# Kernel optimization log

Measured on AMD Instinct MI355X. Metric: run time of the kernel, lower is better.

Reference implementation:

```python
import jax, jax.numpy as jnp
import numpy as np

EPS = 1e-7        # min norm to avoid div-by-zero
BALL_EPS = 1e-5   # Poincare-ball boundary clip


def _norm(x):
    return jnp.maximum(jnp.linalg.norm(x, axis=-1, keepdims=True), EPS)


def expmap0(u, c):
    sc = jnp.sqrt(c)
    n = _norm(u)
    return jnp.tanh(sc * n) * u / (sc * n)


def logmap0(p, c):
    sc = jnp.sqrt(c)
    n = _norm(p)
    return jnp.arctanh(jnp.minimum(sc * n, 1.0 - BALL_EPS)) * p / (sc * n)


def proj(x, c):
    # project onto the ball of radius (1-eps)/sqrt(c)
    n = _norm(x)
    maxn = (1.0 - BALL_EPS) / jnp.sqrt(c)
    return jnp.where(n > maxn, x * (maxn / n), x)


def mobius_matvec(W, x, c):
    # Mobius matrix-vector multiply on the Poincare ball
    sc = jnp.sqrt(c)
    xn = _norm(x)                       # [N,1]
    mx = x @ W                          # [N,D]
    mxn = _norm(mx)
    t = jnp.tanh((mxn / xn) * jnp.arctanh(jnp.minimum(sc * xn, 1.0 - BALL_EPS)))
    return t * mx / (sc * mxn)


def spmm(rows, cols, vals, x):
    # sparse(adj) @ x, adjacency in COO form
    return jax.ops.segment_sum(vals[:, None] * x[cols], rows, num_segments=x.shape[0])


def hgc_layer(x, rows, cols, vals, W, c, c_lin):
    t = logmap0(x, c)                               # to tangent space at origin
    h = proj(mobius_matvec(W, t, c_lin), c_lin)     # LinearHyperbolic (c=1.0, no activation)
    s = spmm(rows, cols, vals, h)                   # HyperbolicAggregation: adj @ h
    agg = proj(expmap0(s, c), c)
    a = jax.nn.relu(logmap0(agg, c))                # ActivationHyperbolic (relu, c_in=c_out=c)
    return proj(expmap0(a, c), c)


def setup_inputs() -> dict:
    key = jax.random.key(0)
    ks = jax.random.split(key, 7)
    N, D, E = 10000, 1433, 100000
    x = jax.random.normal(ks[0], (N, D), jnp.float32) * 0.1  # keep points off the boundary
    rows = jax.random.randint(ks[1], (E,), 0, N)
    cols = jax.random.randint(ks[2], (E,), 0, N)
    vals = jax.random.uniform(ks[3], (E,), jnp.float32) / 10.0  # ~normalized adjacency weights
    scale = 1.0 / np.sqrt(D)
    W0 = jax.random.normal(ks[4], (D, D), jnp.float32) * scale
    W1 = jax.random.normal(ks[5], (D, D), jnp.float32) * scale
    W2 = jax.random.normal(ks[6], (D, D), jnp.float32) * scale
    return {"x": x, "W0": W0, "W1": W1, "W2": W2, "vals": vals, "rows": rows, "cols": cols}


def reference(x, W0, W1, W2, vals, rows, cols):
    c = jnp.float32(0.4)       # c_map == c0 for every layer in the source
    c_lin = jnp.float32(1.0)   # LinearHyperbolic hard-coded c
    h = expmap0(x, c)
    for W in (W0, W1, W2):
        h = hgc_layer(h, rows, cols, vals, W, c, c_lin)
    return h
```

## Files before the change

### kernel.cpp

```cpp
#include <hip/hip_runtime.h>

typedef unsigned short u16;
typedef unsigned int   u32;

#define M_ROWS 10000
#define D_DIM  1433
#define KPAD   1472
#define NPAD   1536
#define MPAD   10240
#define N_EDGE 100000
#define HPAD   1440
#define HP32   720
#define NKT    23
#define EPS    1e-7f
#define BEPS   1e-5f
#define SC     0.6324555320336759f

typedef __bf16 bf16x8 __attribute__((ext_vector_type(8)));
typedef float  f32x4  __attribute__((ext_vector_type(4)));
typedef u32    u32x4  __attribute__((ext_vector_type(4)));

__device__ __forceinline__ u16 f2bf(float f) {
  union { float f; unsigned u; } v; v.f = f;
  unsigned r = v.u + 0x7FFFu + ((v.u >> 16) & 1u);
  return (u16)(r >> 16);
}
__device__ __forceinline__ u32 pack2bf(float lo, float hi) {
  return (u32)f2bf(lo) | ((u32)f2bf(hi) << 16);
}
__device__ __forceinline__ float bflo(u32 u) { return __uint_as_float(u << 16); }
__device__ __forceinline__ float bfhi(u32 u) { return __uint_as_float(u & 0xFFFF0000u); }

__device__ __forceinline__ float atanh_f(float y) {
  return 0.5f * logf((1.f + y) / (1.f - y));
}

__device__ __forceinline__ void gl_lds16(const u16* g, u16* l) {
  __builtin_amdgcn_global_load_lds((const __attribute__((address_space(1))) void*)(const void*)g,
                                   (__attribute__((address_space(3))) void*)(void*)l,
                                   16, 0, 0);
}

__global__ __launch_bounds__(512, 1) void gemm256(
    const u16* __restrict__ A,
    const u16* __restrict__ B,
    u16* __restrict__ C,
    float* __restrict__ nrm)
{
  __shared__ u16 lds[2][2][256 * 64];

  const int tid  = threadIdx.x;
  const int lane = tid & 63;
  const int w    = tid >> 6;
  const int wr   = w >> 2;
  const int wc   = w & 3;

  const int flat = blockIdx.x;
  const int wgid = (flat & 7) * 30 + (flat >> 3);
  const int gy = wgid % 6;
  const int gx = wgid / 6;
  const long arow0 = (long)gx * 256;
  const long brow0 = (long)gy * 256;

  f32x4 acc[8][4] = {};

  const int sr8 = lane >> 3;
  const int scb = ((lane & 7) << 4) ^ (sr8 << 4);

  auto STG_B = [&](int b, int kt) {
    const long k0 = (long)kt * 64 + (scb >> 1);
#pragma unroll
    for (int l = 0; l < 4; ++l) {
      const int r   = l * 64 + w * 8 + sr8;
      const int dst = l * 4096 + w * 512;
      gl_lds16(B + (brow0 + r) * KPAD + k0, &lds[b][1][dst]);
    }
  };
  auto STG_A = [&](int b, int kt, int sel) {
    const long k0 = (long)kt * 64 + (scb >> 1);
#pragma unroll
    for (int li = 0; li < 2; ++li) {
      const int l   = sel + 2 * li;
      const int r   = l * 64 + w * 8 + sr8;
      const int dst = l * 4096 + w * 512;
      gl_lds16(A + (arow0 + r) * KPAD + k0, &lds[b][0][dst]);
    }
  };

  STG_B(0, 0); STG_A(0, 0, 0); STG_A(0, 0, 1);
  asm volatile("s_waitcnt vmcnt(0)" ::: "memory");
  __builtin_amdgcn_s_barrier();

  for (int kt = 0; kt < NKT; ++kt) {
    const int b = kt & 1;
    const bool pf = (kt + 1 < NKT);

    bf16x8 b0[4], b1[4], a0[4], a1[4];
#pragma unroll
    for (int ni = 0; ni < 4; ++ni) {
      const int row = wc * 64 + ni * 16 + (lane & 15);
      const int kb0 = (((lane >> 4) << 4)) ^ ((row & 7) << 4);
      const int kb1 = (64 + ((lane >> 4) << 4)) ^ ((row & 7) << 4);
      b0[ni] = *(const bf16x8*)&lds[b][1][row * 64 + (kb0 >> 1)];
      b1[ni] = *(const bf16x8*)&lds[b][1][row * 64 + (kb1 >> 1)];
    }
#pragma unroll
    for (int ml = 0; ml < 4; ++ml) {
      const int row = wr * 128 + ml * 16 + (lane & 15);
      const int kb0 = (((lane >> 4) << 4)) ^ ((row & 7) << 4);
      const int kb1 = (64 + ((lane >> 4) << 4)) ^ ((row & 7) << 4);
      a0[ml] = *(const bf16x8*)&lds[b][0][row * 64 + (kb0 >> 1)];
      a1[ml] = *(const bf16x8*)&lds[b][0][row * 64 + (kb1 >> 1)];
    }
    if (pf) { STG_B(b ^ 1, kt + 1); STG_A(b ^ 1, kt + 1, 0); }
    __builtin_amdgcn_s_setprio(1);
#pragma unroll
    for (int ml = 0; ml < 4; ++ml)
#pragma unroll
      for (int ni = 0; ni < 4; ++ni)
        acc[ml][ni] = __builtin_amdgcn_mfma_f32_16x16x32_bf16(a0[ml], b0[ni], acc[ml][ni], 0, 0, 0);
#pragma unroll
    for (int ml = 0; ml < 4; ++ml)
#pragma unroll
      for (int ni = 0; ni < 4; ++ni)
        acc[ml][ni] = __builtin_amdgcn_mfma_f32_16x16x32_bf16(a1[ml], b1[ni], acc[ml][ni], 0, 0, 0);
    __builtin_amdgcn_s_setprio(0);
    if (pf) asm volatile("s_waitcnt vmcnt(6)" ::: "memory");
    else    asm volatile("s_waitcnt vmcnt(0)" ::: "memory");
    __builtin_amdgcn_s_barrier();

    bf16x8 c0[4], c1[4];
#pragma unroll
    for (int ml = 0; ml < 4; ++ml) {
      const int row = wr * 128 + (4 + ml) * 16 + (lane & 15);
      const int kb0 = (((lane >> 4) << 4)) ^ ((row & 7) << 4);
      const int kb1 = (64 + ((lane >> 4) << 4)) ^ ((row & 7) << 4);
      c0[ml] = *(const bf16x8*)&lds[b][0][row * 64 + (kb0 >> 1)];
      c1[ml] = *(const bf16x8*)&lds[b][0][row * 64 + (kb1 >> 1)];
    }
    if (pf) STG_A(b ^ 1, kt + 1, 1);
    __builtin_amdgcn_s_setprio(1);
#pragma unroll
    for (int ml = 0; ml < 4; ++ml)
#pragma unroll
      for (int ni = 0; ni < 4; ++ni)
        acc[4 + ml][ni] = __builtin_amdgcn_mfma_f32_16x16x32_bf16(c0[ml], b0[ni], acc[4 + ml][ni], 0, 0, 0);
#pragma unroll
    for (int ml = 0; ml < 4; ++ml)
#pragma unroll
      for (int ni = 0; ni < 4; ++ni)
        acc[4 + ml][ni] = __builtin_amdgcn_mfma_f32_16x16x32_bf16(c1[ml], b1[ni], acc[4 + ml][ni], 0, 0, 0);
    __builtin_amdgcn_s_setprio(0);
    if (pf) asm volatile("s_waitcnt vmcnt(2)" ::: "memory");
    __builtin_amdgcn_s_barrier();
  }

  const int orw = (lane >> 4) * 4;
  const int ocl = lane & 15;

#pragma unroll
  for (int mi = 0; mi < 8; ++mi)
#pragma unroll
    for (int r = 0; r < 4; ++r) {
      float s = 0.f;
#pragma unroll
      for (int ni = 0; ni < 4; ++ni) {
        const long j = brow0 + wc * 64 + ni * 16 + ocl;
        const float v = acc[mi][ni][r];
        s += (j < D_DIM) ? v * v : 0.f;
      }
      s += __shfl_xor(s, 1, 64);
      s += __shfl_xor(s, 2, 64);
      s += __shfl_xor(s, 4, 64);
      s += __shfl_xor(s, 8, 64);
      if ((lane & 15) == 0)
        atomicAdd(&nrm[arow0 + wr * 128 + mi * 16 + orw + r], s);
    }

#pragma unroll
  for (int mi = 0; mi < 8; ++mi) {
    const long i0 = arow0 + wr * 128 + mi * 16 + orw;
    if (i0 >= M_ROWS) continue;
#pragma unroll
    for (int ni = 0; ni < 4; ++ni) {
      const long j = brow0 + wc * 64 + ni * 16 + ocl;
      if (j >= HPAD) continue;
#pragma unroll
      for (int r = 0; r < 4; ++r) {
        const long i = i0 + r;
        if (i < M_ROWS) C[i * HPAD + j] = (j < D_DIM) ? f2bf(acc[mi][ni][r]) : (u16)0;
      }
    }
  }
}

__device__ __forceinline__ float2 block_reduce2(float a, float b) {
  __shared__ float sa[4], sb[4];
#pragma unroll
  for (int off = 32; off > 0; off >>= 1) {
    a += __shfl_down(a, off, 64);
    b += __shfl_down(b, off, 64);
  }
  const int tid = threadIdx.x;
  if ((tid & 63) == 0) { sa[tid >> 6] = a; sb[tid >> 6] = b; }
  __syncthreads();
  const float ra = sa[0] + sa[1] + sa[2] + sa[3];
  const float rb = sb[0] + sb[1] + sb[2] + sb[3];
  __syncthreads();
  return make_float2(ra, rb);
}

__global__ __launch_bounds__(256) void pre_k(const float* __restrict__ x,
                                             u16* __restrict__ t,
                                             float* __restrict__ xn) {
  const long i = blockIdx.x;
  const int tid = threadIdx.x;
  u16* trow = t + i * KPAD;
  if (i >= M_ROWS) {
#pragma unroll
    for (int jj = 0; jj < 6; ++jj) { int j = tid + jj * 256; if (j < KPAD) trow[j] = 0; }
    return;
  }
  const float* xr = x + i * D_DIM;
  float v[6]; float s2 = 0.f;
#pragma unroll
  for (int jj = 0; jj < 6; ++jj) {
    int j = tid + jj * 256;
    v[jj] = (j < D_DIM) ? xr[j] : 0.f;
    s2 += v[jj] * v[jj];
  }
  s2 = block_reduce2(s2, 0.f).x;
  const float nx_t = sqrtf(s2);
  const float nx   = fmaxf(nx_t, EPS);
  const float al   = tanhf(SC * nx) / (SC * nx);
  const float n1   = fmaxf(al * nx_t, EPS);
  const float be   = atanh_f(fminf(SC * n1, 1.f - BEPS)) / (SC * n1);
  const float sca  = al * be;
  if (tid == 0) xn[i] = fmaxf(sca * nx_t, EPS);
#pragma unroll
  for (int jj = 0; jj < 6; ++jj) {
    int j = tid + jj * 256;
    if (j < KPAD) trow[j] = (j < D_DIM) ? f2bf(sca * v[jj]) : (u16)0;
  }
}

__global__ void zero_f(float* p, int n) {
  int i = blockIdx.x * 256 + threadIdx.x;
  if (i < n) p[i] = 0.f;
}

__global__ void fold_k(const int* __restrict__ ecol, const float* __restrict__ eval,
                       const float* __restrict__ nrm, const float* __restrict__ xn,
                       u32* __restrict__ pe, int E) {
  const int e = blockIdx.x * 256 + threadIdx.x;
  if (e >= E) return;
  const int c = ecol[e];
  const float realn = sqrtf(nrm[c]);
  const float mxn   = fmaxf(realn, EPS);
  const float xi    = xn[c];
  const float tf    = tanhf((mxn / xi) * atanh_f(fminf(xi, 1.f - BEPS)));
  float S = tf / mxn;
  const float hn = fmaxf(S * realn, EPS);
  const float maxn = 1.f - BEPS;
  if (hn > maxn) S *= maxn / hn;
  pe[e] = ((u32)c << 16) | (u32)f2bf(eval[e] * S);
}

__global__ __launch_bounds__(256) void spmm_post(const int* __restrict__ rp,
                                                 const u32* __restrict__ pe,
                                                 const u32* __restrict__ mxp,
                                                 u16* __restrict__ t,
                                                 float* __restrict__ xn,
                                                 float* __restrict__ out,
                                                 const int last) {
  const long r = blockIdx.x;
  const int tid = threadIdx.x;
  if (r >= M_ROWS) {
    if (!last && tid < 184) {
      u32* trow32 = (u32*)(t + r * KPAD);
#pragma unroll
      for (int k = 0; k < 4; ++k) trow32[4 * tid + k] = 0u;
    }
    return;
  }
  const bool act = tid < 180;
  const long boff = 4 * tid;
  float a[8] = {0.f, 0.f, 0.f, 0.f, 0.f, 0.f, 0.f, 0.f};
  const int e0 = rp[r], e1 = rp[r + 1];
  for (int e = e0; e < e1; e += 12) {
    u32 pp[12]; float w[12];
#pragma unroll
    for (int j = 0; j < 12; ++j) {
      const int ee = e + j;
      const int ec = (ee < e1) ? ee : (e1 - 1);
      pp[j] = pe[ec];
      w[j]  = (ee < e1) ? bflo(pp[j]) : 0.f;
    }
    if (act) {
      u32x4 q[12];
#pragma unroll
      for (int j = 0; j < 12; ++j)
        q[j] = *(const u32x4*)&mxp[(long)(pp[j] >> 16) * HP32 + boff];
#pragma unroll
      for (int j = 0; j < 12; ++j) {
#pragma unroll
        for (int k = 0; k < 4; ++k) {
          a[2 * k]     += w[j] * bflo(q[j][k]);
          a[2 * k + 1] += w[j] * bfhi(q[j][k]);
        }
      }
    }
  }
  float s2 = 0.f, s2p = 0.f;
#pragma unroll
  for (int k = 0; k < 8; ++k) {
    const int col = 8 * tid + k;
    const float v = (act && col < D_DIM) ? a[k] : 0.f;
    a[k] = v;
    s2 += v * v;
    const float p = fmaxf(v, 0.f);
    s2p += p * p;
  }
  const float2 red = block_reduce2(s2, s2p);
  const float ns_t  = sqrtf(red.x);
  const float nsp_t = sqrtf(red.y);
  const float maxn = (1.f - BEPS) / SC;
  const float ns = fmaxf(ns_t, EPS);
  const float al = tanhf(SC * ns) / (SC * ns);
  const float n1 = fmaxf(al * ns_t, EPS);
  const float be = (n1 > maxn) ? (maxn / n1) : 1.f;
  const float n2 = fmaxf(be * al * ns_t, EPS);
  const float lam = atanh_f(fminf(SC * n2, 1.f - BEPS)) / (SC * n2);
  const float g = lam * be * al;
  const float na_t = g * nsp_t;
  const float n3 = fmaxf(na_t, EPS);
  const float mu = tanhf(SC * n3) / (SC * n3);
  const float n4 = fmaxf(mu * na_t, EPS);
  const float nu = (n4 > maxn) ? (maxn / n4) : 1.f;
  const float T = nu * mu * g;
  if (last) {
    if (act) {
      float* orow = out + r * (long)D_DIM;
#pragma unroll
      for (int k = 0; k < 8; ++k) {
        const int col = 8 * tid + k;
        if (col < D_DIM) orow[col] = T * fmaxf(a[k], 0.f);
      }
    }
  } else {
    const float nh_t = T * nsp_t;
    const float n5 = fmaxf(nh_t, EPS);
    const float kap = atanh_f(fminf(SC * n5, 1.f - BEPS)) / (SC * n5);
    const float F = kap * T;
    if (tid == 0) xn[r] = fmaxf(F * nsp_t, EPS);
    u32* trow32 = (u32*)(t + r * KPAD);
    if (act) {
#pragma unroll
      for (int k = 0; k < 4; ++k)
        trow32[4 * tid + k] = pack2bf(F * fmaxf(a[2 * k], 0.f), F * fmaxf(a[2 * k + 1], 0.f));
    } else if (tid < 184) {
#pragma unroll
      for (int k = 0; k < 4; ++k) trow32[4 * tid + k] = 0u;
    }
  }
}

__global__ void wt_conv(const float* __restrict__ W, u16* __restrict__ Wt) {
  __shared__ float tile[32][33];
  const int kb = blockIdx.x * 32, nb = blockIdx.y * 32;
  const int tx = threadIdx.x, ty = threadIdx.y;
#pragma unroll
  for (int r = 0; r < 32; r += 8) {
    const int k = kb + ty + r, n = nb + tx;
    tile[ty + r][tx] = (k < D_DIM && n < D_DIM) ? W[(long)k * D_DIM + n] : 0.f;
  }
  __syncthreads();
#pragma unroll
  for (int r = 0; r < 32; r += 8) {
    const int n = nb + ty + r, k = kb + tx;
    if (n < NPAD && k < KPAD) Wt[(long)n * KPAD + k] = f2bf(tile[tx][ty + r]);
  }
}

__global__ void zero_int(int* p, int n) {
  int i = blockIdx.x * 256 + threadIdx.x;
  if (i < n) p[i] = 0;
}
__global__ void hist_k(const int* __restrict__ rows, int* __restrict__ counts, int E) {
  int e = blockIdx.x * 256 + threadIdx.x;
  if (e < E) atomicAdd(&counts[rows[e]], 1);
}
__global__ __launch_bounds__(1024) void scan_rp(const int* __restrict__ counts,
                                                int* __restrict__ rp, int n) {
  __shared__ int sd[1024];
  __shared__ int carry_s;
  const int tid = threadIdx.x;
  if (tid == 0) { carry_s = 0; rp[0] = 0; }
  __syncthreads();
  for (int base = 0; base < n; base += 1024) {
    const int i = base + tid;
    sd[tid] = (i < n) ? counts[i] : 0;
    __syncthreads();
    for (int off = 1; off < 1024; off <<= 1) {
      const int tv = (tid >= off) ? sd[tid - off] : 0;
      __syncthreads();
      sd[tid] += tv;
      __syncthreads();
    }
    const int carry = carry_s;
    if (i < n) rp[i + 1] = carry + sd[tid];
    __syncthreads();
    if (tid == 1023) carry_s = carry + sd[1023];
    __syncthreads();
  }
}
__global__ void scatter_k(const int* __restrict__ rows, const int* __restrict__ cols,
                          const float* __restrict__ vals, const int* __restrict__ rp,
                          int* __restrict__ cursor, int* __restrict__ ecol,
                          float* __restrict__ eval, int E) {
  int e = blockIdx.x * 256 + threadIdx.x;
  if (e < E) {
    const int r = rows[e];
    const int pos = rp[r] + atomicAdd(&cursor[r], 1);
    ecol[pos] = cols[e];
    eval[pos] = vals[e];
  }
}

extern "C" void kernel_launch(void* const* d_in, const int* in_sizes, int n_in,
                              void* d_out, int out_size, void* d_ws, size_t ws_size,
                              hipStream_t stream) {
  (void)in_sizes; (void)n_in; (void)out_size; (void)ws_size;
  const float* x    = (const float*)d_in[0];
  const float* W[3] = {(const float*)d_in[1], (const float*)d_in[2], (const float*)d_in[3]};
  const float* vals = (const float*)d_in[4];
  const int*   rows = (const int*)d_in[5];
  const int*   cols = (const int*)d_in[6];
  float* out = (float*)d_out;

  char* base = (char*)d_ws;
  size_t off = 0;
  auto take = [&](size_t bytes) {
    void* q = base + off;
    off = (off + bytes + 255) & ~(size_t)255;
    return q;
  };
  u16*   t    = (u16*)take((size_t)MPAD * KPAD * 2);
  u16*   Wt   = (u16*)take((size_t)NPAD * KPAD * 2);
  u16*   mx   = (u16*)take((size_t)M_ROWS * HPAD * 2);
  float* nrm3 = (float*)take((size_t)3 * MPAD * 4);
  float* xn   = (float*)take((size_t)M_ROWS * 4);
  int*   cnt  = (int*)take((size_t)M_ROWS * 2 * 4);
  int*   rp   = (int*)take((size_t)(M_ROWS + 1) * 4);
  int*   ecol = (int*)take((size_t)N_EDGE * 4);
  float* eval = (float*)take((size_t)N_EDGE * 4);
  u32*   pe   = (u32*)take((size_t)N_EDGE * 4);

  zero_int<<<(2 * M_ROWS + 255) / 256, 256, 0, stream>>>(cnt, 2 * M_ROWS);
  hist_k<<<(N_EDGE + 255) / 256, 256, 0, stream>>>(rows, cnt, N_EDGE);
  scan_rp<<<1, 1024, 0, stream>>>(cnt, rp, M_ROWS);
  scatter_k<<<(N_EDGE + 255) / 256, 256, 0, stream>>>(rows, cols, vals, rp,
                                                      cnt + M_ROWS, ecol, eval, N_EDGE);
  zero_f<<<(3 * MPAD + 255) / 256, 256, 0, stream>>>(nrm3, 3 * MPAD);

  pre_k<<<MPAD, 256, 0, stream>>>(x, t, xn);

  for (int L = 0; L < 3; ++L) {
    float* nrm = nrm3 + (size_t)L * MPAD;
    wt_conv<<<dim3(46, 48), dim3(32, 8), 0, stream>>>(W[L], Wt);
    gemm256<<<240, 512, 0, stream>>>(t, Wt, mx, nrm);
    fold_k<<<(N_EDGE + 255) / 256, 256, 0, stream>>>(ecol, eval, nrm, xn, pe, N_EDGE);
    spmm_post<<<MPAD, 256, 0, stream>>>(rp, pe, (const u32*)mx, t, xn, out, (L == 2) ? 1 : 0);
  }
}
```

Baseline: 369.5 us.

## Restructure GEMM main loop into four quadrant phases with two-stage-ahead prefetch

The GEMM k-loop now splits each 256x256 tile step into four MFMA quadrant phases. B and A loads are issued in half-tile pieces two k-steps ahead, reusing the current buffer as soon as its fragments have been read into registers, to hide global-load latency better than single-step double buffering. Separately, spmm_post now runs with 192 threads instead of 256, since only 180 threads do work, and the block reduction is templated on wave count. The tighter schedule adds more barriers and relies on vmcnt counts being exactly right, so a miscount could race on LDS.

```diff
diff --git a/kernel.cpp b/kernel.cpp
--- a/kernel.cpp
+++ b/kernel.cpp
@@ -41,6 +41,8 @@
                                    16, 0, 0);
 }
 
+#define BAR() asm volatile("s_barrier" ::: "memory")
+
 __global__ __launch_bounds__(512, 1) void gemm256(
     const u16* __restrict__ A,
     const u16* __restrict__ B,
@@ -66,93 +68,137 @@
 
   const int sr8 = lane >> 3;
   const int scb = ((lane & 7) << 4) ^ (sr8 << 4);
-
-  auto STG_B = [&](int b, int kt) {
-    const long k0 = (long)kt * 64 + (scb >> 1);
-#pragma unroll
-    for (int l = 0; l < 4; ++l) {
-      const int r   = l * 64 + w * 8 + sr8;
-      const int dst = l * 4096 + w * 512;
-      gl_lds16(B + (brow0 + r) * KPAD + k0, &lds[b][1][dst]);
-    }
-  };
+  const int l15 = lane & 15;
+  const int khi = (lane >> 4) << 4;
+
   auto STG_A = [&](int b, int kt, int sel) {
     const long k0 = (long)kt * 64 + (scb >> 1);
 #pragma unroll
     for (int li = 0; li < 2; ++li) {
-      const int l   = sel + 2 * li;
-      const int r   = l * 64 + w * 8 + sr8;
+      const int l = sel + 2 * li;
+      const int r = l * 64 + w * 8 + sr8;
       const int dst = l * 4096 + w * 512;
       gl_lds16(A + (arow0 + r) * KPAD + k0, &lds[b][0][dst]);
     }
   };
-
-  STG_B(0, 0); STG_A(0, 0, 0); STG_A(0, 0, 1);
-  asm volatile("s_waitcnt vmcnt(0)" ::: "memory");
-  __builtin_amdgcn_s_barrier();
+  auto STG_B = [&](int b, int kt, int half) {
+    const long k0 = (long)kt * 64 + (scb >> 1);
+#pragma unroll
+    for (int j = 0; j < 2; ++j) {
+      const int r128 = j * 64 + w * 8;
+      const int rb   = ((r128 >> 5) << 6) + half * 32 + (r128 & 31);
+      gl_lds16(B + (brow0 + rb + sr8) * KPAD + k0, &lds[b][1][rb * 64]);
+    }
+  };
+
+  STG_B(0, 0, 0); STG_A(0, 0, 0); STG_B(0, 0, 1); STG_A(0, 0, 1);
+  STG_A(1, 1, 0); STG_B(1, 1, 1); STG_A(1, 1, 1);
+  asm volatile("s_waitcnt vmcnt(6)" ::: "memory");
+  BAR();
 
   for (int kt = 0; kt < NKT; ++kt) {
     const int b = kt & 1;
-    const bool pf = (kt + 1 < NKT);
-
-    bf16x8 b0[4], b1[4], a0[4], a1[4];
-#pragma unroll
-    for (int ni = 0; ni < 4; ++ni) {
-      const int row = wc * 64 + ni * 16 + (lane & 15);
-      const int kb0 = (((lane >> 4) << 4)) ^ ((row & 7) << 4);
-      const int kb1 = (64 + ((lane >> 4) << 4)) ^ ((row & 7) << 4);
-      b0[ni] = *(const bf16x8*)&lds[b][1][row * 64 + (kb0 >> 1)];
-      b1[ni] = *(const bf16x8*)&lds[b][1][row * 64 + (kb1 >> 1)];
-    }
-#pragma unroll
-    for (int ml = 0; ml < 4; ++ml) {
-      const int row = wr * 128 + ml * 16 + (lane & 15);
-      const int kb0 = (((lane >> 4) << 4)) ^ ((row & 7) << 4);
-      const int kb1 = (64 + ((lane >> 4) << 4)) ^ ((row & 7) << 4);
-      a0[ml] = *(const bf16x8*)&lds[b][0][row * 64 + (kb0 >> 1)];
-      a1[ml] = *(const bf16x8*)&lds[b][0][row * 64 + (kb1 >> 1)];
-    }
-    if (pf) { STG_B(b ^ 1, kt + 1); STG_A(b ^ 1, kt + 1, 0); }
+    const bool s1 = (kt + 1 < NKT);
+    const bool s2 = (kt + 2 < NKT);
+
+    bf16x8 a0[4], a1[4], bl0[2], bl1[2];
+#pragma unroll
+    for (int mi = 0; mi < 4; ++mi) {
+      const int row = wr * 128 + mi * 16 + l15;
+      const int x0 = (khi) ^ ((row & 7) << 4);
+      const int x1 = (64 + khi) ^ ((row & 7) << 4);
+      a0[mi] = *(const bf16x8*)&lds[b][0][row * 64 + (x0 >> 1)];
+      a1[mi] = *(const bf16x8*)&lds[b][0][row * 64 + (x1 >> 1)];
+    }
+#pragma unroll
+    for (int ni = 0; ni < 2; ++ni) {
+      const int row = wc * 64 + ni * 16 + l15;
+      const int x0 = (khi) ^ ((row & 7) << 4);
+      const int x1 = (64 + khi) ^ ((row & 7) << 4);
+      bl0[ni] = *(const bf16x8*)&lds[b][1][row * 64 + (x0 >> 1)];
+      bl1[ni] = *(const bf16x8*)&lds[b][1][row * 64 + (x1 >> 1)];
+    }
+    if (s1) STG_B(b ^ 1, kt + 1, 0);
+    BAR();
     __builtin_amdgcn_s_setprio(1);
 #pragma unroll
-    for (int ml = 0; ml < 4; ++ml)
-#pragma unroll
-      for (int ni = 0; ni < 4; ++ni)
-        acc[ml][ni] = __builtin_amdgcn_mfma_f32_16x16x32_bf16(a0[ml], b0[ni], acc[ml][ni], 0, 0, 0);
-#pragma unroll
-    for (int ml = 0; ml < 4; ++ml)
-#pragma unroll
-      for (int ni = 0; ni < 4; ++ni)
-        acc[ml][ni] = __builtin_amdgcn_mfma_f32_16x16x32_bf16(a1[ml], b1[ni], acc[ml][ni], 0, 0, 0);
+    for (int mi = 0; mi < 4; ++mi)
+#pragma unroll
+      for (int ni = 0; ni < 2; ++ni)
+        acc[mi][ni] = __builtin_amdgcn_mfma_f32_16x16x32_bf16(a0[mi], bl0[ni], acc[mi][ni], 0, 0, 0);
+#pragma unroll
+    for (int mi = 0; mi < 4; ++mi)
+#pragma unroll
+      for (int ni = 0; ni < 2; ++ni)
+        acc[mi][ni] = __builtin_amdgcn_mfma_f32_16x16x32_bf16(a1[mi], bl1[ni], acc[mi][ni], 0, 0, 0);
     __builtin_amdgcn_s_setprio(0);
-    if (pf) asm volatile("s_waitcnt vmcnt(6)" ::: "memory");
-    else    asm volatile("s_waitcnt vmcnt(0)" ::: "memory");
-    __builtin_amdgcn_s_barrier();
-
-    bf16x8 c0[4], c1[4];
-#pragma unroll
-    for (int ml = 0; ml < 4; ++ml) {
-      const int row = wr * 128 + (4 + ml) * 16 + (lane & 15);
-      const int kb0 = (((lane >> 4) << 4)) ^ ((row & 7) << 4);
-      const int kb1 = (64 + ((lane >> 4) << 4)) ^ ((row & 7) << 4);
-      c0[ml] = *(const bf16x8*)&lds[b][0][row * 64 + (kb0 >> 1)];
-      c1[ml] = *(const bf16x8*)&lds[b][0][row * 64 + (kb1 >> 1)];
-    }
-    if (pf) STG_A(b ^ 1, kt + 1, 1);
+    BAR();
+
+    bf16x8 bh0[2], bh1[2];
+#pragma unroll
+    for (int ni = 0; ni < 2; ++ni) {
+      const int row = wc * 64 + (2 + ni) * 16 + l15;
+      const int x0 = (khi) ^ ((row & 7) << 4);
+      const int x1 = (64 + khi) ^ ((row & 7) << 4);
+      bh0[ni] = *(const bf16x8*)&lds[b][1][row * 64 + (x0 >> 1)];
+      bh1[ni] = *(const bf16x8*)&lds[b][1][row * 64 + (x1 >> 1)];
+    }
+    if (s2) STG_A(b, kt + 2, 0);
+    BAR();
     __builtin_amdgcn_s_setprio(1);
 #pragma unroll
-    for (int ml = 0; ml < 4; ++ml)
-#pragma unroll
-      for (int ni = 0; ni < 4; ++ni)
-        acc[4 + ml][ni] = __builtin_amdgcn_mfma_f32_16x16x32_bf16(c0[ml], b0[ni], acc[4 + ml][ni], 0, 0, 0);
-#pragma unroll
-    for (int ml = 0; ml < 4; ++ml)
-#pragma unroll
-      for (int ni = 0; ni < 4; ++ni)
-        acc[4 + ml][ni] = __builtin_amdgcn_mfma_f32_16x16x32_bf16(c1[ml], b1[ni], acc[4 + ml][ni], 0, 0, 0);
+    for (int mi = 0; mi < 4; ++mi)
+#pragma unroll
+      for (int ni = 0; ni < 2; ++ni)
+        acc[mi][2 + ni] = __builtin_amdgcn_mfma_f32_16x16x32_bf16(a0[mi], bh0[ni], acc[mi][2 + ni], 0, 0, 0);
+#pragma unroll
+    for (int mi = 0; mi < 4; ++mi)
+#pragma unroll
+      for (int ni = 0; ni < 2; ++ni)
+        acc[mi][2 + ni] = __builtin_amdgcn_mfma_f32_16x16x32_bf16(a1[mi], bh1[ni], acc[mi][2 + ni], 0, 0, 0);
     __builtin_amdgcn_s_setprio(0);
-    if (pf) asm volatile("s_waitcnt vmcnt(2)" ::: "memory");
-    __builtin_amdgcn_s_barrier();
+    BAR();
+
+#pragma unroll
+    for (int mi = 0; mi < 4; ++mi) {
+      const int row = wr * 128 + (4 + mi) * 16 + l15;
+      const int x0 = (khi) ^ ((row & 7) << 4);
+      const int x1 = (64 + khi) ^ ((row & 7) << 4);
+      a0[mi] = *(const bf16x8*)&lds[b][0][row * 64 + (x0 >> 1)];
+      a1[mi] = *(const bf16x8*)&lds[b][0][row * 64 + (x1 >> 1)];
+    }
+    if (s2) STG_B(b, kt + 2, 1);
+    BAR();
+    __builtin_amdgcn_s_setprio(1);
+#pragma unroll
+    for (int mi = 0; mi < 4; ++mi)
+#pragma unroll
+      for (int ni = 0; ni < 2; ++ni)
+        acc[4 + mi][2 + ni] = __builtin_amdgcn_mfma_f32_16x16x32_bf16(a0[mi], bh0[ni], acc[4 + mi][2 + ni], 0, 0, 0);
+#pragma unroll
+    for (int mi = 0; mi < 4; ++mi)
+#pragma unroll
+      for (int ni = 0; ni < 2; ++ni)
+        acc[4 + mi][2 + ni] = __builtin_amdgcn_mfma_f32_16x16x32_bf16(a1[mi], bh1[ni], acc[4 + mi][2 + ni], 0, 0, 0);
+    __builtin_amdgcn_s_setprio(0);
+    BAR();
+
+    if (s2) STG_A(b, kt + 2, 1);
+    __builtin_amdgcn_s_setprio(1);
+#pragma unroll
+    for (int mi = 0; mi < 4; ++mi)
+#pragma unroll
+      for (int ni = 0; ni < 2; ++ni)
+        acc[4 + mi][ni] = __builtin_amdgcn_mfma_f32_16x16x32_bf16(a0[mi], bl0[ni], acc[4 + mi][ni], 0, 0, 0);
+#pragma unroll
+    for (int mi = 0; mi < 4; ++mi)
+#pragma unroll
+      for (int ni = 0; ni < 2; ++ni)
+        acc[4 + mi][ni] = __builtin_amdgcn_mfma_f32_16x16x32_bf16(a1[mi], bl1[ni], acc[4 + mi][ni], 0, 0, 0);
+    __builtin_amdgcn_s_setprio(0);
+    if (s2)      asm volatile("s_waitcnt vmcnt(6)" ::: "memory");
+    else if (s1) asm volatile("s_waitcnt vmcnt(0)" ::: "memory");
+    BAR();
   }
 
   const int orw = (lane >> 4) * 4;
@@ -194,8 +240,9 @@
   }
 }
 
+template<int NW>
 __device__ __forceinline__ float2 block_reduce2(float a, float b) {
-  __shared__ float sa[4], sb[4];
+  __shared__ float sa[NW], sb[NW];
 #pragma unroll
   for (int off = 32; off > 0; off >>= 1) {
     a += __shfl_down(a, off, 64);
@@ -204,8 +251,9 @@
   const int tid = threadIdx.x;
   if ((tid & 63) == 0) { sa[tid >> 6] = a; sb[tid >> 6] = b; }
   __syncthreads();
-  const float ra = sa[0] + sa[1] + sa[2] + sa[3];
-  const float rb = sb[0] + sb[1] + sb[2] + sb[3];
+  float ra = 0.f, rb = 0.f;
+#pragma unroll
+  for (int i = 0; i < NW; ++i) { ra += sa[i]; rb += sb[i]; }
   __syncthreads();
   return make_float2(ra, rb);
 }
@@ -229,7 +277,7 @@
     v[jj] = (j < D_DIM) ? xr[j] : 0.f;
     s2 += v[jj] * v[jj];
   }
-  s2 = block_reduce2(s2, 0.f).x;
+  s2 = block_reduce2<4>(s2, 0.f).x;
   const float nx_t = sqrtf(s2);
   const float nx   = fmaxf(nx_t, EPS);
   const float al   = tanhf(SC * nx) / (SC * nx);
@@ -266,7 +314,7 @@
   pe[e] = ((u32)c << 16) | (u32)f2bf(eval[e] * S);
 }
 
-__global__ __launch_bounds__(256) void spmm_post(const int* __restrict__ rp,
+__global__ __launch_bounds__(192) void spmm_post(const int* __restrict__ rp,
                                                  const u32* __restrict__ pe,
                                                  const u32* __restrict__ mxp,
                                                  u16* __restrict__ t,
@@ -321,7 +369,7 @@
     const float p = fmaxf(v, 0.f);
     s2p += p * p;
   }
-  const float2 red = block_reduce2(s2, s2p);
+  const float2 red = block_reduce2<3>(s2, s2p);
   const float ns_t  = sqrtf(red.x);
   const float nsp_t = sqrtf(red.y);
   const float maxn = (1.f - BEPS) / SC;
@@ -470,6 +518,6 @@
     wt_conv<<<dim3(46, 48), dim3(32, 8), 0, stream>>>(W[L], Wt);
     gemm256<<<240, 512, 0, stream>>>(t, Wt, mx, nrm);
     fold_k<<<(N_EDGE + 255) / 256, 256, 0, stream>>>(ecol, eval, nrm, xn, pe, N_EDGE);
-    spmm_post<<<MPAD, 256, 0, stream>>>(rp, pe, (const u32*)mx, t, xn, out, (L == 2) ? 1 : 0);
-  }
-}
+    spmm_post<<<MPAD, 192, 0, stream>>>(rp, pe, (const u32*)mx, t, xn, out, (L == 2) ? 1 : 0);
+  }
+}
```

After: 376.3 us. No clear change (+1.9%).

## Interleave GEMM LDS reads with prefetch via sched groups; shrink spmm blocks to 192

Applied to the files above, without the earlier changes.

Restructures the GEMM main loop: the last k-tile is peeled out so the prefetch branches disappear, LDS fragment reads are split around the global-to-LDS prefetch issue, and sched_group_barrier hints are added to interleave DS reads, VMEM and MFMA. The aim is to hide LDS and global latency behind MFMA work. Separately, spmm_post now launches 192 threads instead of 256, since only 180 lanes were active, and the block reduction is templated on wave count. The scheduling hints may constrain the compiler poorly and raise register pressure.

```diff
diff --git a/kernel.cpp b/kernel.cpp
--- a/kernel.cpp
+++ b/kernel.cpp
@@ -41,6 +41,9 @@
                                    16, 0, 0);
 }
 
+#define BAR() asm volatile("s_barrier" ::: "memory")
+#define SGB(m, n) __builtin_amdgcn_sched_group_barrier((m), (n), 0)
+
 __global__ __launch_bounds__(512, 1) void gemm256(
     const u16* __restrict__ A,
     const u16* __restrict__ B,
@@ -66,6 +69,8 @@
 
   const int sr8 = lane >> 3;
   const int scb = ((lane & 7) << 4) ^ (sr8 << 4);
+  const int l15 = lane & 15;
+  const int khi = (lane >> 4) << 4;
 
   auto STG_B = [&](int b, int kt) {
     const long k0 = (long)kt * 64 + (scb >> 1);
@@ -89,70 +94,143 @@
 
   STG_B(0, 0); STG_A(0, 0, 0); STG_A(0, 0, 1);
   asm volatile("s_waitcnt vmcnt(0)" ::: "memory");
-  __builtin_amdgcn_s_barrier();
-
-  for (int kt = 0; kt < NKT; ++kt) {
+  BAR();
+
+  for (int kt = 0; kt < NKT - 1; ++kt) {
     const int b = kt & 1;
-    const bool pf = (kt + 1 < NKT);
-
-    bf16x8 b0[4], b1[4], a0[4], a1[4];
+
+    bf16x8 a0[4], a1[4], b0q[4], b1q[4];
 #pragma unroll
     for (int ni = 0; ni < 4; ++ni) {
-      const int row = wc * 64 + ni * 16 + (lane & 15);
-      const int kb0 = (((lane >> 4) << 4)) ^ ((row & 7) << 4);
-      const int kb1 = (64 + ((lane >> 4) << 4)) ^ ((row & 7) << 4);
-      b0[ni] = *(const bf16x8*)&lds[b][1][row * 64 + (kb0 >> 1)];
-      b1[ni] = *(const bf16x8*)&lds[b][1][row * 64 + (kb1 >> 1)];
+      const int row = wc * 64 + ni * 16 + l15;
+      const int x0 = (khi) ^ ((row & 7) << 4);
+      b0q[ni] = *(const bf16x8*)&lds[b][1][row * 64 + (x0 >> 1)];
     }
 #pragma unroll
     for (int ml = 0; ml < 4; ++ml) {
-      const int row = wr * 128 + ml * 16 + (lane & 15);
-      const int kb0 = (((lane >> 4) << 4)) ^ ((row & 7) << 4);
-      const int kb1 = (64 + ((lane >> 4) << 4)) ^ ((row & 7) << 4);
-      a0[ml] = *(const bf16x8*)&lds[b][0][row * 64 + (kb0 >> 1)];
-      a1[ml] = *(const bf16x8*)&lds[b][0][row * 64 + (kb1 >> 1)];
-    }
-    if (pf) { STG_B(b ^ 1, kt + 1); STG_A(b ^ 1, kt + 1, 0); }
+      const int row = wr * 128 + ml * 16 + l15;
+      const int x0 = (khi) ^ ((row & 7) << 4);
+      a0[ml] = *(const bf16x8*)&lds[b][0][row * 64 + (x0 >> 1)];
+    }
+    STG_B(b ^ 1, kt + 1);
+    STG_A(b ^ 1, kt + 1, 0);
+#pragma unroll
+    for (int ni = 0; ni < 4; ++ni) {
+      const int row = wc * 64 + ni * 16 + l15;
+      const int x1 = (64 + khi) ^ ((row & 7) << 4);
+      b1q[ni] = *(const bf16x8*)&lds[b][1][row * 64 + (x1 >> 1)];
+    }
+#pragma unroll
+    for (int ml = 0; ml < 4; ++ml) {
+      const int row = wr * 128 + ml * 16 + l15;
+      const int x1 = (64 + khi) ^ ((row & 7) << 4);
+      a1[ml] = *(const bf16x8*)&lds[b][0][row * 64 + (x1 >> 1)];
+    }
     __builtin_amdgcn_s_setprio(1);
 #pragma unroll
     for (int ml = 0; ml < 4; ++ml)
 #pragma unroll
       for (int ni = 0; ni < 4; ++ni)
-        acc[ml][ni] = __builtin_amdgcn_mfma_f32_16x16x32_bf16(a0[ml], b0[ni], acc[ml][ni], 0, 0, 0);
-#pragma unroll
-    for (int ml = 0; ml < 4; ++ml)
-#pragma unroll
-      for (int ni = 0; ni < 4; ++ni)
-        acc[ml][ni] = __builtin_amdgcn_mfma_f32_16x16x32_bf16(a1[ml], b1[ni], acc[ml][ni], 0, 0, 0);
+        acc[ml][ni] = __builtin_amdgcn_mfma_f32_16x16x32_bf16(a0[ml], b0q[ni], acc[ml][ni], 0, 0, 0);
+#pragma unroll
+    for (int ml = 0; ml < 4; ++ml)
+#pragma unroll
+      for (int ni = 0; ni < 4; ++ni)
+        acc[ml][ni] = __builtin_amdgcn_mfma_f32_16x16x32_bf16(a1[ml], b1q[ni], acc[ml][ni], 0, 0, 0);
     __builtin_amdgcn_s_setprio(0);
-    if (pf) asm volatile("s_waitcnt vmcnt(6)" ::: "memory");
-    else    asm volatile("s_waitcnt vmcnt(0)" ::: "memory");
-    __builtin_amdgcn_s_barrier();
+    SGB(0x100, 8);
+    SGB(0x010, 6);
+    SGB(0x008, 16);
+    SGB(0x100, 8);
+    SGB(0x008, 16);
+    asm volatile("s_waitcnt vmcnt(6)" ::: "memory");
+    BAR();
 
     bf16x8 c0[4], c1[4];
 #pragma unroll
     for (int ml = 0; ml < 4; ++ml) {
-      const int row = wr * 128 + (4 + ml) * 16 + (lane & 15);
-      const int kb0 = (((lane >> 4) << 4)) ^ ((row & 7) << 4);
-      const int kb1 = (64 + ((lane >> 4) << 4)) ^ ((row & 7) << 4);
-      c0[ml] = *(const bf16x8*)&lds[b][0][row * 64 + (kb0 >> 1)];
-      c1[ml] = *(const bf16x8*)&lds[b][0][row * 64 + (kb1 >> 1)];
-    }
-    if (pf) STG_A(b ^ 1, kt + 1, 1);
+      const int row = wr * 128 + (4 + ml) * 16 + l15;
+      const int x0 = (khi) ^ ((row & 7) << 4);
+      c0[ml] = *(const bf16x8*)&lds[b][0][row * 64 + (x0 >> 1)];
+    }
+    STG_A(b ^ 1, kt + 1, 1);
+#pragma unroll
+    for (int ml = 0; ml < 4; ++ml) {
+      const int row = wr * 128 + (4 + ml) * 16 + l15;
+      const int x1 = (64 + khi) ^ ((row & 7) << 4);
+      c1[ml] = *(const bf16x8*)&lds[b][0][row * 64 + (x1 >> 1)];
+    }
     __builtin_amdgcn_s_setprio(1);
 #pragma unroll
     for (int ml = 0; ml < 4; ++ml)
 #pragma unroll
       for (int ni = 0; ni < 4; ++ni)
-        acc[4 + ml][ni] = __builtin_amdgcn_mfma_f32_16x16x32_bf16(c0[ml], b0[ni], acc[4 + ml][ni], 0, 0, 0);
-#pragma unroll
-    for (int ml = 0; ml < 4; ++ml)
-#pragma unroll
-      for (int ni = 0; ni < 4; ++ni)
-        acc[4 + ml][ni] = __builtin_amdgcn_mfma_f32_16x16x32_bf16(c1[ml], b1[ni], acc[4 + ml][ni], 0, 0, 0);
+        acc[4 + ml][ni] = __builtin_amdgcn_mfma_f32_16x16x32_bf16(c0[ml], b0q[ni], acc[4 + ml][ni], 0, 0, 0);
+#pragma unroll
+    for (int ml = 0; ml < 4; ++ml)
+#pragma unroll
+      for (int ni = 0; ni < 4; ++ni)
+        acc[4 + ml][ni] = __builtin_amdgcn_mfma_f32_16x16x32_bf16(c1[ml], b1q[ni], acc[4 + ml][ni], 0, 0, 0);
     __builtin_amdgcn_s_setprio(0);
-    if (pf) asm volatile("s_waitcnt vmcnt(2)" ::: "memory");
-    __builtin_amdgcn_s_barrier();
+    SGB(0x100, 4);
+    SGB(0x010, 2);
+    SGB(0x008, 16);
+    SGB(0x100, 4);
+    SGB(0x008, 16);
+    asm volatile("s_waitcnt vmcnt(2)" ::: "memory");
+    BAR();
+  }
+
+  {
+    const int b = (NKT - 1) & 1;
+    bf16x8 a0[4], a1[4], b0q[4], b1q[4];
+#pragma unroll
+    for (int ni = 0; ni < 4; ++ni) {
+      const int row = wc * 64 + ni * 16 + l15;
+      const int x0 = (khi) ^ ((row & 7) << 4);
+      const int x1 = (64 + khi) ^ ((row & 7) << 4);
+      b0q[ni] = *(const bf16x8*)&lds[b][1][row * 64 + (x0 >> 1)];
+      b1q[ni] = *(const bf16x8*)&lds[b][1][row * 64 + (x1 >> 1)];
+    }
+#pragma unroll
+    for (int ml = 0; ml < 4; ++ml) {
+      const int row = wr * 128 + ml * 16 + l15;
+      const int x0 = (khi) ^ ((row & 7) << 4);
+      const int x1 = (64 + khi) ^ ((row & 7) << 4);
+      a0[ml] = *(const bf16x8*)&lds[b][0][row * 64 + (x0 >> 1)];
+      a1[ml] = *(const bf16x8*)&lds[b][0][row * 64 + (x1 >> 1)];
+    }
+#pragma unroll
+    for (int ml = 0; ml < 4; ++ml)
+#pragma unroll
+      for (int ni = 0; ni < 4; ++ni)
+        acc[ml][ni] = __builtin_amdgcn_mfma_f32_16x16x32_bf16(a0[ml], b0q[ni], acc[ml][ni], 0, 0, 0);
+#pragma unroll
+    for (int ml = 0; ml < 4; ++ml)
+#pragma unroll
+      for (int ni = 0; ni < 4; ++ni)
+        acc[ml][ni] = __builtin_amdgcn_mfma_f32_16x16x32_bf16(a1[ml], b1q[ni], acc[ml][ni], 0, 0, 0);
+    asm volatile("s_waitcnt vmcnt(0)" ::: "memory");
+    BAR();
+    bf16x8 c0[4], c1[4];
+#pragma unroll
+    for (int ml = 0; ml < 4; ++ml) {
+      const int row = wr * 128 + (4 + ml) * 16 + l15;
+      const int x0 = (khi) ^ ((row & 7) << 4);
+      const int x1 = (64 + khi) ^ ((row & 7) << 4);
+      c0[ml] = *(const bf16x8*)&lds[b][0][row * 64 + (x0 >> 1)];
+      c1[ml] = *(const bf16x8*)&lds[b][0][row * 64 + (x1 >> 1)];
+    }
+#pragma unroll
+    for (int ml = 0; ml < 4; ++ml)
+#pragma unroll
+      for (int ni = 0; ni < 4; ++ni)
+        acc[4 + ml][ni] = __builtin_amdgcn_mfma_f32_16x16x32_bf16(c0[ml], b0q[ni], acc[4 + ml][ni], 0, 0, 0);
+#pragma unroll
+    for (int ml = 0; ml < 4; ++ml)
+#pragma unroll
+      for (int ni = 0; ni < 4; ++ni)
+        acc[4 + ml][ni] = __builtin_amdgcn_mfma_f32_16x16x32_bf16(c1[ml], b1q[ni], acc[4 + ml][ni], 0, 0, 0);
   }
 
   const int orw = (lane >> 4) * 4;
@@ -194,8 +272,9 @@
   }
 }
 
+template<int NW>
 __device__ __forceinline__ float2 block_reduce2(float a, float b) {
-  __shared__ float sa[4], sb[4];
+  __shared__ float sa[NW], sb[NW];
 #pragma unroll
   for (int off = 32; off > 0; off >>= 1) {
     a += __shfl_down(a, off, 64);
@@ -204,8 +283,9 @@
   const int tid = threadIdx.x;
   if ((tid & 63) == 0) { sa[tid >> 6] = a; sb[tid >> 6] = b; }
   __syncthreads();
-  const float ra = sa[0] + sa[1] + sa[2] + sa[3];
-  const float rb = sb[0] + sb[1] + sb[2] + sb[3];
+  float ra = 0.f, rb = 0.f;
+#pragma unroll
+  for (int i = 0; i < NW; ++i) { ra += sa[i]; rb += sb[i]; }
   __syncthreads();
   return make_float2(ra, rb);
 }
@@ -229,7 +309,7 @@
     v[jj] = (j < D_DIM) ? xr[j] : 0.f;
     s2 += v[jj] * v[jj];
   }
-  s2 = block_reduce2(s2, 0.f).x;
+  s2 = block_reduce2<4>(s2, 0.f).x;
   const float nx_t = sqrtf(s2);
   const float nx   = fmaxf(nx_t, EPS);
   const float al   = tanhf(SC * nx) / (SC * nx);
@@ -266,7 +346,7 @@
   pe[e] = ((u32)c << 16) | (u32)f2bf(eval[e] * S);
 }
 
-__global__ __launch_bounds__(256) void spmm_post(const int* __restrict__ rp,
+__global__ __launch_bounds__(192) void spmm_post(const int* __restrict__ rp,
                                                  const u32* __restrict__ pe,
                                                  const u32* __restrict__ mxp,
                                                  u16* __restrict__ t,
@@ -321,7 +401,7 @@
     const float p = fmaxf(v, 0.f);
     s2p += p * p;
   }
-  const float2 red = block_reduce2(s2, s2p);
+  const float2 red = block_reduce2<3>(s2, s2p);
   const float ns_t  = sqrtf(red.x);
   const float nsp_t = sqrtf(red.y);
   const float maxn = (1.f - BEPS) / SC;
@@ -470,6 +550,6 @@
     wt_conv<<<dim3(46, 48), dim3(32, 8), 0, stream>>>(W[L], Wt);
     gemm256<<<240, 512, 0, stream>>>(t, Wt, mx, nrm);
     fold_k<<<(N_EDGE + 255) / 256, 256, 0, stream>>>(ecol, eval, nrm, xn, pe, N_EDGE);
-    spmm_post<<<MPAD, 256, 0, stream>>>(rp, pe, (const u32*)mx, t, xn, out, (L == 2) ? 1 : 0);
-  }
-}
+    spmm_post<<<MPAD, 192, 0, stream>>>(rp, pe, (const u32*)mx, t, xn, out, (L == 2) ? 1 : 0);
+  }
+}
```

Result: no change. 372.7 us (+0.9%).
